# Performance work log

Measured on AMD Instinct MI355X. Metric: run time of the kernel, lower is better.

The kernel has to match this reference:

```python
import jax, jax.numpy as jnp
import numpy as np

N, N_H = 256, 64          # detections per image, humans (permuted to top)
NUM_ITER = 2
E = 1024                   # node_encoding_size == box_feature_size
T_LIS, K_LIS, W_LIS = 8.3, 12.0, 10.0


def lis(x):
    # Low-grade Instance Suppression
    return T_LIS / (1.0 + jnp.exp(K_LIS - W_LIS * x))


def setup_inputs() -> dict:
    key = jax.random.key(0)
    ks = jax.random.split(key, 25)
    s = 0.02  # weight scale keeps sigmoid/relu in a sane range
    rn = lambda k, shape, sc=1.0: jax.random.normal(k, shape, jnp.float32) * sc
    inp = {}
    inp['box_features'] = rn(ks[0], (N, 12544))            # [N, 256*7*7]
    inp['node_spatial'] = rn(ks[1], (N, 1024))             # conv spatial-head output
    inp['scores'] = jax.random.uniform(ks[2], (N,), jnp.float32)
    labels = jax.random.randint(ks[3], (N,), 1, 80)
    inp['labels'] = labels.at[:N_H].set(0)                 # humans (idx 0) on top
    inp['class_mask'] = jax.random.bernoulli(ks[4], 0.2, (80, 117))
    inp['W_bh1'] = rn(ks[5], (12544, 1024), s); inp['b_bh1'] = jnp.zeros((1024,), jnp.float32)
    inp['W_bh2'] = rn(ks[6], (1024, 1024), s);  inp['b_bh2'] = jnp.zeros((1024,), jnp.float32)
    inp['W_sa']  = rn(ks[7], (1024, 1024), s)
    inp['W_a1']  = rn(ks[8], (4096, 2048), s); inp['b_a1'] = jnp.zeros((2048,), jnp.float32)
    inp['W_a2']  = rn(ks[9], (2048, 1024), s); inp['b_a2'] = jnp.zeros((1024,), jnp.float32)
    inp['W_a3']  = rn(ks[10], (1024, 1), s);   inp['b_a3'] = jnp.zeros((1,), jnp.float32)
    inp['W_hm']  = rn(ks[11], (1024, 1024), s); inp['b_hm'] = jnp.zeros((1024,), jnp.float32)
    inp['W_om']  = rn(ks[12], (1024, 1024), s); inp['b_om'] = jnp.zeros((1024,), jnp.float32)
    inp['W_hu']  = rn(ks[13], (2048, 1024), s)
    inp['W_ou']  = rn(ks[14], (2048, 1024), s)
    return inp


def _keep_indices():
    xv, yv = np.meshgrid(np.arange(N_H), np.arange(N), indexing='ij')
    m = (xv != yv).ravel()
    return jnp.asarray(xv.ravel()[m]), jnp.asarray(yv.ravel()[m])


def reference(box_features, node_spatial, scores, W_bh1, b_bh1, W_bh2, b_bh2,
              W_sa, W_a1, b_a1, W_a2, b_a2, W_a3, b_a3,
              W_hm, b_hm, W_om, b_om, W_hu, W_ou, labels, class_mask):
    # box_head: Flatten -> Linear -> ReLU -> Linear -> ReLU
    enc = jax.nn.relu(box_features @ W_bh1 + b_bh1)
    enc = jax.nn.relu(enc @ W_bh2 + b_bh2)                 # [N, E]
    h_enc = enc[:N_H]                                      # [N_H, E]
    h_sp = node_spatial[:N_H]                              # [N_H, 1024]
    # spatial_attention on pairwise spatial differences (fixed across iters)
    diff = node_spatial[None, :, :] - h_sp[:, None, :]     # [N_H, N, 1024]
    h_to_o = jnp.einsum('hnd,de->hne', diff, W_sa)         # Linear, no bias
    o_to_h = -h_to_o
    adj = jnp.ones((N_H, N), enc.dtype)
    for _ in range(NUM_ITER):
        # adjacency MLP + sigmoid over all n_h*n pairs
        hf = jnp.concatenate([h_enc, h_sp], axis=1)        # [N_H, 2048]
        of = jnp.concatenate([enc, node_spatial], axis=1)  # [N, 2048]
        pair_in = jnp.concatenate([
            jnp.broadcast_to(hf[:, None, :], (N_H, N, 2 * E)),
            jnp.broadcast_to(of[None, :, :], (N_H, N, 2 * E))], axis=-1)  # [N_H,N,4096]
        hdn = jax.nn.relu(pair_in @ W_a1 + b_a1)
        hdn = jax.nn.relu(hdn @ W_a2 + b_a2)
        adj = jax.nn.sigmoid((hdn @ W_a3 + b_a3)[..., 0])  # [N_H, N]
        # object -> human messages
        obj_msg = jax.nn.relu(enc @ W_om + b_om)           # [N, R]
        agg_o = (adj[..., None] * (obj_msg[None, :, :] * o_to_h)).sum(1)  # [N_H, R]
        h_enc = jnp.concatenate([h_enc, agg_o], axis=1) @ W_hu            # [N_H, E]
        # human -> object messages
        hum_msg = jax.nn.relu(h_enc @ W_hm + b_hm)         # [N_H, R]
        agg_h = (adj[..., None] * (hum_msg[:, None, :] * h_to_o)).sum(0)  # [N, R]
        enc = jnp.concatenate([enc, agg_h], axis=1) @ W_ou                # [N, E]
    x_keep, y_keep = _keep_indices()                       # [P], P = N_H*N - N_H
    pair_feats = jnp.concatenate([h_enc[x_keep], h_sp[x_keep],
                                  enc[y_keep], node_spatial[y_keep]], axis=1)  # [P, 4096]
    # prior scores: LIS(score_h)*LIS(score_o) scattered to valid target classes
    prod = lis(scores[x_keep]) * lis(scores[y_keep])       # [P]
    prior = prod[:, None] * class_mask[labels[y_keep]].astype(pair_feats.dtype)  # [P, 117]
    prior = adj[x_keep, y_keep][:, None] * prior
    return jnp.concatenate([pair_feats, prior], axis=1)    # [P, 4096+117]
```

## Files before the change

kernel.cpp:

```cpp
#include <hip/hip_runtime.h>

using bf16 = __bf16;
typedef __bf16 bf16x4 __attribute__((ext_vector_type(4)));
typedef __bf16 bf16x8 __attribute__((ext_vector_type(8)));
typedef float  f32x4  __attribute__((ext_vector_type(4)));

#define GST 40

__device__ __forceinline__ float ldf(const void* p, size_t i, int f32) {
    return f32 ? ((const float*)p)[i] : (float)((const bf16*)p)[i];
}
__device__ __forceinline__ bf16x8 ld8(const void* p, size_t i, int f32) {
    bf16x8 r;
    if (f32) {
        f32x4 a = *(const f32x4*)((const float*)p + i);
        f32x4 b = *(const f32x4*)((const float*)p + i + 4);
#pragma unroll
        for (int j = 0; j < 4; ++j) { r[j] = (bf16)a[j]; r[j + 4] = (bf16)b[j]; }
    } else {
        r = *(const bf16x8*)((const bf16*)p + i);
    }
    return r;
}
__device__ __forceinline__ void st1(void* p, size_t i, float v, int f32) {
    if (f32) ((float*)p)[i] = v;
    else     ((bf16*)p)[i] = (bf16)v;
}

__device__ __forceinline__ void gl_lds16(const bf16* g, bf16* l) {
    __builtin_amdgcn_global_load_lds(
        (const __attribute__((address_space(1))) void*)g,
        (__attribute__((address_space(3))) void*)l, 16, 0, 0);
}

__global__ void init_flag(int* __restrict__ dflag) { *dflag = 0; }

__global__ void detect_kernel(const unsigned short* __restrict__ p, int n,
                              int* __restrict__ dflag)
{
    const unsigned int* q = (const unsigned int*)p;
    const int nw = n >> 1;
    int hit = 0;
    for (int i = blockIdx.x * 256 + threadIdx.x; i < nw; i += gridDim.x * 256) {
        unsigned int w = q[i];
        if ((w & 0x7F80u) == 0x7F80u || (w & 0x7F800000u) == 0x7F800000u) hit = 1;
    }
    if (__any(hit) && (threadIdx.x & 63) == 0) atomicOr(dflag, 1);
}

__global__ void cvt_kernel(const void* __restrict__ src, bf16* __restrict__ dst,
                           int n, const int* __restrict__ dflag)
{
    const int f32 = *dflag;
    const int stride = gridDim.x * 256;
    const int nv = n >> 3;
    for (int i = blockIdx.x * 256 + threadIdx.x; i < nv; i += stride) {
        bf16x8 v = ld8(src, (size_t)i * 8, f32);
        *(bf16x8*)(dst + (size_t)i * 8) = v;
    }
}

__global__ void cvt_smalls(const void* b_bh1, const void* b_bh2, const void* b_om,
                           const void* b_hm, const void* b_a1, const void* b_a2,
                           const void* w_a3, const void* b_a3, const void* scores,
                           bf16* __restrict__ smalls, const int* __restrict__ dflag)
{
    const int f32 = *dflag;
    int i = blockIdx.x * 256 + threadIdx.x;
    const void* s; int off;
    if      (i < 1024) { s = b_bh1; off = 0;    }
    else if (i < 2048) { s = b_bh2; off = 1024; }
    else if (i < 3072) { s = b_om;  off = 2048; }
    else if (i < 4096) { s = b_hm;  off = 3072; }
    else if (i < 6144) { s = b_a1;  off = 4096; }
    else if (i < 7168) { s = b_a2;  off = 6144; }
    else if (i < 8192) { s = w_a3;  off = 7168; }
    else if (i < 8193) { s = b_a3;  off = 8192; }
    else if (i >= 8208 && i < 8464) { s = scores; off = 8208; }
    else return;
    smalls[i] = (bf16)ldf(s, i - off, f32);
}

__global__ void transpose_any(const void* __restrict__ W, bf16* __restrict__ Wt,
                              int K, int N, const int* __restrict__ dflag)
{
    __shared__ bf16 tile[32][33];
    const int f32 = *dflag;
    const int n0 = blockIdx.x * 32, k0 = blockIdx.y * 32;
    const int tx = threadIdx.x, ty = threadIdx.y;
#pragma unroll
    for (int i = 0; i < 4; ++i)
        tile[ty + i * 8][tx] = (bf16)ldf(W, (size_t)(k0 + ty + i * 8) * N + n0 + tx, f32);
    __syncthreads();
#pragma unroll
    for (int i = 0; i < 4; ++i)
        Wt[(size_t)(n0 + ty + i * 8) * K + k0 + tx] = tile[tx][ty + i * 8];
}

__global__ __launch_bounds__(256)
void gemm_p(const bf16* __restrict__ A, int lda,
            const void* __restrict__ B, size_t boff, int ldb,
            float* __restrict__ part, int N, int Kc,
            const int* __restrict__ dflag)
{
    __shared__ bf16 As[64 * GST];
    __shared__ bf16 Bs[64 * GST];
    const int f32 = *dflag;
    const int t = threadIdx.x;
    const int l = t & 63;
    const int quad = l >> 4, lr = l & 15;
    const int w = t >> 6, wm = w >> 1, wn = w & 1;
    const int mBlock = blockIdx.y * 64, nBlock = blockIdx.x * 64;
    const int ar = t >> 2, ac = (t & 3) * 8;
    const int kr = t >> 3, nc = (t & 7) * 8;
    const int kBeg = blockIdx.z * Kc;
    const int nIter = Kc >> 5;

    f32x4 acc[2][2] = {};

    bf16x8 avr = *(const bf16x8*)(A + (size_t)(mBlock + ar) * lda + kBeg + ac);
    bf16x8 bvr = ld8(B, boff + (size_t)(kBeg + kr) * ldb + nBlock + nc, f32);

    for (int it = 0; it < nIter; ++it) {
        *(bf16x8*)&As[ar * GST + ac] = avr;
#pragma unroll
        for (int j = 0; j < 8; ++j) {
            int wr = nc + j;
            Bs[wr * GST + (kr ^ (((wr >> 3) & 3) << 3))] = bvr[j];
        }
        __syncthreads();
        if (it + 1 < nIter) {
            int k0 = kBeg + (it + 1) * 32;
            avr = *(const bf16x8*)(A + (size_t)(mBlock + ar) * lda + k0 + ac);
            bvr = ld8(B, boff + (size_t)(k0 + kr) * ldb + nBlock + nc, f32);
        }
        bf16x8 af[2], bfr[2];
#pragma unroll
        for (int mi = 0; mi < 2; ++mi)
            af[mi] = *(const bf16x8*)&As[(wm * 32 + mi * 16 + lr) * GST + quad * 8];
#pragma unroll
        for (int nj = 0; nj < 2; ++nj) {
            int row = wn * 32 + nj * 16 + lr;
            bfr[nj] = *(const bf16x8*)&Bs[row * GST + ((quad * 8) ^ (((row >> 3) & 3) << 3))];
        }
#pragma unroll
        for (int mi = 0; mi < 2; ++mi)
#pragma unroll
            for (int nj = 0; nj < 2; ++nj)
                acc[mi][nj] = __builtin_amdgcn_mfma_f32_16x16x32_bf16(
                    af[mi], bfr[nj], acc[mi][nj], 0, 0, 0);
        __syncthreads();
    }

    float* outp = part + (size_t)blockIdx.z * ((size_t)gridDim.y * 64 * N);
#pragma unroll
    for (int mi = 0; mi < 2; ++mi)
#pragma unroll
        for (int nj = 0; nj < 2; ++nj) {
            int col = nBlock + wn * 32 + nj * 16 + lr;
#pragma unroll
            for (int rr = 0; rr < 4; ++rr) {
                int row = mBlock + wm * 32 + mi * 16 + quad * 4 + rr;
                outp[(size_t)row * N + col] = acc[mi][nj][rr];
            }
        }
}

template<bool RELU, bool BIAS, bool F32OUT>
__global__ void reduce_k(const float* __restrict__ part, int S, int total,
                         const bf16* __restrict__ bias, void* __restrict__ out, int N)
{
    int base = (blockIdx.x * 256 + threadIdx.x) * 4;
    if (base >= total) return;
    f32x4 s = *(const f32x4*)(part + base);
    for (int z = 1; z < S; ++z) {
        f32x4 v = *(const f32x4*)(part + (size_t)z * total + base);
        s[0] += v[0]; s[1] += v[1]; s[2] += v[2]; s[3] += v[3];
    }
    int col = base % N;
#pragma unroll
    for (int j = 0; j < 4; ++j) {
        float v = s[j];
        if (BIAS) v += (float)bias[col + j];
        if (RELU) v = fmaxf(v, 0.f);
        if (F32OUT) ((float*)out)[base + j] = v;
        else        ((bf16*)out)[base + j] = (bf16)v;
    }
}

__global__ void build_pairA(const float* __restrict__ Hb, const float* __restrict__ Op,
                            bf16* __restrict__ A)
{
    const int n = blockIdx.x;
    const int h = blockIdx.y;
    const int k = threadIdx.x * 8;
    const float* hp = Hb + (size_t)h * 2048 + k;
    const float* op = Op + (size_t)n * 2048 + k;
    f32x4 h0 = *(const f32x4*)hp, h1 = *(const f32x4*)(hp + 4);
    f32x4 o0 = *(const f32x4*)op, o1 = *(const f32x4*)(op + 4);
    bf16x8 r;
#pragma unroll
    for (int j = 0; j < 4; ++j) {
        r[j]     = (bf16)fmaxf(h0[j] + o0[j], 0.f);
        r[j + 4] = (bf16)fmaxf(h1[j] + o1[j], 0.f);
    }
    *(bf16x8*)(A + ((size_t)h * 256 + n) * 2048 + k) = r;
}

__global__ __launch_bounds__(256)
void pair_gemm(const bf16* __restrict__ Apg, const bf16* __restrict__ Wt_a2,
               const bf16* __restrict__ b_a2, const bf16* __restrict__ w_a3,
               float* __restrict__ slots)
{
    __shared__ bf16 As[128 * 32];
    __shared__ bf16 Bs[128 * 32];
    const int t = threadIdx.x;
    const int l = t & 63, w = t >> 6;
    const int quad = l >> 4, lr = l & 15;
    const int wm = w >> 1, wn = w & 1;
    const int nb = blockIdx.x, mb = blockIdx.y;
    const int p0 = mb * 128;

    const int grow = w * 16 + (l >> 2);
    const int slot = l & 3;
    const int csrc = slot ^ ((grow >> 1) & 3);
    const bf16* Asrc0 = Apg + (size_t)(p0 + grow) * 2048 + csrc * 8;
    const bf16* Asrc1 = Apg + (size_t)(p0 + 64 + grow) * 2048 + csrc * 8;
    const bf16* Bsrc0 = Wt_a2 + (size_t)(nb * 128 + grow) * 2048 + csrc * 8;
    const bf16* Bsrc1 = Wt_a2 + (size_t)(nb * 128 + 64 + grow) * 2048 + csrc * 8;
    bf16* AsW0 = As + w * 512;
    bf16* AsW1 = As + 2048 + w * 512;
    bf16* BsW0 = Bs + w * 512;
    bf16* BsW1 = Bs + 2048 + w * 512;

    f32x4 acc[4][4] = {};

    for (int k0 = 0; k0 < 2048; k0 += 32) {
        gl_lds16(Asrc0 + k0, AsW0);
        gl_lds16(Asrc1 + k0, AsW1);
        gl_lds16(Bsrc0 + k0, BsW0);
        gl_lds16(Bsrc1 + k0, BsW1);
        __syncthreads();

        bf16x8 af[4], bfr[4];
#pragma unroll
        for (int mi = 0; mi < 4; ++mi) {
            int row = wm * 64 + mi * 16 + lr;
            int sl = quad ^ ((row >> 1) & 3);
            af[mi] = *(const bf16x8*)&As[row * 32 + sl * 8];
        }
#pragma unroll
        for (int nj = 0; nj < 4; ++nj) {
            int row = wn * 64 + nj * 16 + lr;
            int sl = quad ^ ((row >> 1) & 3);
            bfr[nj] = *(const bf16x8*)&Bs[row * 32 + sl * 8];
        }
#pragma unroll
        for (int mi = 0; mi < 4; ++mi)
#pragma unroll
            for (int nj = 0; nj < 4; ++nj)
                acc[mi][nj] = __builtin_amdgcn_mfma_f32_16x16x32_bf16(
                    af[mi], bfr[nj], acc[mi][nj], 0, 0, 0);
        __syncthreads();
    }

    float w3v[4], b2v[4];
#pragma unroll
    for (int nj = 0; nj < 4; ++nj) {
        int col = nb * 128 + wn * 64 + nj * 16 + lr;
        w3v[nj] = (float)w_a3[col];
        b2v[nj] = (float)b_a2[col];
    }
#pragma unroll
    for (int mi = 0; mi < 4; ++mi) {
        f32x4 rs = {0.f, 0.f, 0.f, 0.f};
#pragma unroll
        for (int nj = 0; nj < 4; ++nj)
#pragma unroll
            for (int rr = 0; rr < 4; ++rr)
                rs[rr] += fmaxf(acc[mi][nj][rr] + b2v[nj], 0.f) * w3v[nj];
#pragma unroll
        for (int off = 1; off < 16; off <<= 1) {
            rs[0] += __shfl_xor(rs[0], off);
            rs[1] += __shfl_xor(rs[1], off);
            rs[2] += __shfl_xor(rs[2], off);
            rs[3] += __shfl_xor(rs[3], off);
        }
        if (lr == 0) {
            int p = p0 + wm * 64 + mi * 16 + quad * 4;
            int slot2 = nb * 2 + wn;
            slots[(size_t)(p + 0) * 16 + slot2] = rs[0];
            slots[(size_t)(p + 1) * 16 + slot2] = rs[1];
            slots[(size_t)(p + 2) * 16 + slot2] = rs[2];
            slots[(size_t)(p + 3) * 16 + slot2] = rs[3];
        }
    }
}

__global__ void adj_finalize(const float* __restrict__ slots,
                             const bf16* __restrict__ b_a3, float* __restrict__ adj)
{
    int i = blockIdx.x * 256 + threadIdx.x;
    float s = (float)b_a3[0];
#pragma unroll
    for (int k = 0; k < 16; ++k) s += slots[(size_t)i * 16 + k];
    adj[i] = 1.f / (1.f + expf(-s));
}

__global__ void copy_rows(const bf16* __restrict__ src, int lds_,
                          bf16* __restrict__ dst, int ldd)
{
    int c = blockIdx.x * 256 + threadIdx.x;
    int r = blockIdx.y;
    dst[(size_t)r * ldd + c] = src[(size_t)r * lds_ + c];
}

__global__ void concat2(const bf16* __restrict__ L, const bf16* __restrict__ R,
                        bf16* __restrict__ dst)
{
    int c = blockIdx.x * 256 + threadIdx.x;
    int r = blockIdx.y;
    dst[(size_t)r * 2048 + c] = (c < 1024) ? L[(size_t)r * 1024 + c]
                                           : R[(size_t)r * 1024 + (c - 1024)];
}

__global__ void agg_o_kernel(const float* __restrict__ adj, const bf16* __restrict__ obj_msg,
                             const bf16* __restrict__ nsW, const bf16* __restrict__ h_enc,
                             bf16* __restrict__ out)
{
    int bx = blockIdx.x;
    int h = blockIdx.y;
    int e = (bx & 3) * 256 + threadIdx.x;
    if (bx < 4) {
        out[(size_t)h * 2048 + e] = h_enc[(size_t)h * 1024 + e];
        return;
    }
    float nh = (float)nsW[h * 1024 + e];
    float s = 0.f;
    for (int n = 0; n < 256; ++n) {
        float a  = adj[h * 256 + n];
        float om = (float)obj_msg[n * 1024 + e];
        float nw = (float)nsW[n * 1024 + e];
        s += a * om * (nh - nw);
    }
    out[(size_t)h * 2048 + 1024 + e] = (bf16)s;
}

__global__ void agg_h_kernel(const float* __restrict__ adj, const bf16* __restrict__ hum_msg,
                             const bf16* __restrict__ nsW, const bf16* __restrict__ enc,
                             bf16* __restrict__ out)
{
    int bx = blockIdx.x;
    int n = blockIdx.y;
    int e = (bx & 3) * 256 + threadIdx.x;
    if (bx < 4) {
        out[(size_t)n * 2048 + e] = enc[(size_t)n * 1024 + e];
        return;
    }
    float nn = (float)nsW[n * 1024 + e];
    float s = 0.f;
    for (int h = 0; h < 64; ++h) {
        float a  = adj[h * 256 + n];
        float hm = (float)hum_msg[h * 1024 + e];
        float nw = (float)nsW[h * 1024 + e];
        s += a * hm * (nn - nw);
    }
    out[(size_t)n * 2048 + 1024 + e] = (bf16)s;
}

__global__ void out_kernel(const bf16* __restrict__ h_enc, const bf16* __restrict__ enc,
                           const bf16* __restrict__ nsp_bf, const float* __restrict__ adj,
                           const bf16* __restrict__ scores_bf, const int* __restrict__ labels,
                           const int* __restrict__ cmask, void* __restrict__ out,
                           const int* __restrict__ dflag)
{
    const int f32 = *dflag;
    const int r = blockIdx.x;
    const int x = r / 255;
    const int tt = r % 255;
    const int y = tt + (tt >= x ? 1 : 0);
    const size_t rbase = (size_t)r * 4213;
    const bf16* seg[4] = { h_enc + x * 1024, nsp_bf + x * 1024, enc + y * 1024, nsp_bf + y * 1024 };
    const int t = threadIdx.x;

    float sx = (float)scores_bf[x], sy = (float)scores_bf[y];
    float lx = 8.3f / (1.f + expf(12.f - 10.f * sx));
    float ly = 8.3f / (1.f + expf(12.f - 10.f * sy));
    float pf = adj[x * 256 + y] * lx * ly;
    const int* cm = cmask + labels[y] * 117;

    auto getv = [&](int e) -> float {
        if (e < 4096) return (float)seg[e >> 10][e & 1023];
        return cm[e - 4096] ? pf : 0.f;
    };

    if (f32) {
        float* op = (float*)out + rbase;
        const int ali = (int)((4 - (rbase & 3)) & 3);
        const int nv = (4213 - ali) >> 2;
        for (int vi = t; vi < nv; vi += 256) {
            int e0 = ali + vi * 4;
            f32x4 v = { getv(e0), getv(e0 + 1), getv(e0 + 2), getv(e0 + 3) };
            *(f32x4*)(op + e0) = v;
        }
        if (t < ali) op[t] = getv(t);
        int te = ali + nv * 4;
        if (t < 4213 - te) op[te + t] = getv(te + t);
    } else {
        bf16* op = (bf16*)out + rbase;
        for (int e = t; e < 4213; e += 256) op[e] = (bf16)getv(e);
    }
}

extern "C" void kernel_launch(void* const* d_in, const int* in_sizes, int n_in,
                              void* d_out, int out_size, void* d_ws, size_t ws_size,
                              hipStream_t stream)
{
    (void)in_sizes; (void)n_in; (void)out_size; (void)ws_size;
    const void* box    = d_in[0];
    const void* nsp    = d_in[1];
    const void* scores = d_in[2];
    const int*  labels = (const int*)d_in[3];
    const int*  cmask  = (const int*)d_in[4];
    const void* W_bh1 = d_in[5],  *b_bh1 = d_in[6];
    const void* W_bh2 = d_in[7],  *b_bh2 = d_in[8];
    const void* W_sa  = d_in[9];
    const void* W_a1  = d_in[10], *b_a1  = d_in[11];
    const void* W_a2  = d_in[12], *b_a2  = d_in[13];
    const void* W_a3  = d_in[14], *b_a3  = d_in[15];
    const void* W_hm  = d_in[16], *b_hm  = d_in[17];
    const void* W_om  = d_in[18], *b_om  = d_in[19];
    const void* W_hu  = d_in[20];
    const void* W_ou  = d_in[21];

    char* ws = (char*)d_ws;
    size_t off = 0;
    auto alloc = [&](size_t bytes) -> void* {
        off = (off + 255) & ~(size_t)255;
        void* p = ws + off;
        off += bytes;
        return p;
    };
    int*  dflag   = (int*)alloc(4);
    bf16* box_bf  = (bf16*)alloc((size_t)256 * 12544 * 2);
    bf16* nsp_bf  = (bf16*)alloc((size_t)256 * 1024 * 2);
    bf16* Wt_a2   = (bf16*)alloc((size_t)1024 * 2048 * 2);
    bf16* smalls  = (bf16*)alloc((size_t)8464 * 2);
    bf16* sb_bh1 = smalls,        *sb_bh2 = smalls + 1024;
    bf16* sb_om  = smalls + 2048, *sb_hm  = smalls + 3072;
    bf16* sb_a1  = smalls + 4096, *sb_a2  = smalls + 6144;
    bf16* sw_a3  = smalls + 7168, *sb_a3  = smalls + 8192;
    bf16* sscore = smalls + 8208;
    bf16* t0      = (bf16*)alloc((size_t)256 * 1024 * 2);
    bf16* enc     = (bf16*)alloc((size_t)256 * 1024 * 2);
    bf16* nsW     = (bf16*)alloc((size_t)256 * 1024 * 2);
    bf16* h_enc   = (bf16*)alloc((size_t)64 * 1024 * 2);
    bf16* hf      = (bf16*)alloc((size_t)64 * 2048 * 2);
    bf16* of      = (bf16*)alloc((size_t)256 * 2048 * 2);
    float* Hpart  = (float*)alloc((size_t)64 * 2048 * 4);
    float* Opart  = (float*)alloc((size_t)256 * 2048 * 4);
    float* slots  = (float*)alloc((size_t)16384 * 16 * 4);
    float* adj    = (float*)alloc((size_t)16384 * 4);
    bf16* obj_msg = (bf16*)alloc((size_t)256 * 1024 * 2);
    bf16* hu_in   = (bf16*)alloc((size_t)64 * 2048 * 2);
    bf16* hum_msg = (bf16*)alloc((size_t)64 * 1024 * 2);
    bf16* ou_in   = (bf16*)alloc((size_t)256 * 2048 * 2);
    float* part   = (float*)alloc((size_t)2097152 * 4);
    bf16* A_bf    = (bf16*)alloc((size_t)16384 * 2048 * 2);

    init_flag<<<1, 1, 0, stream>>>(dflag);
    detect_kernel<<<256, 256, 0, stream>>>((const unsigned short*)box, 524288, dflag);

    cvt_kernel<<<1568, 256, 0, stream>>>(box, box_bf, 256 * 12544, dflag);
    cvt_kernel<<<128, 256, 0, stream>>>(nsp, nsp_bf, 256 * 1024, dflag);
    cvt_smalls<<<34, 256, 0, stream>>>(b_bh1, b_bh2, b_om, b_hm, b_a1, b_a2,
                                       W_a3, b_a3, scores, smalls, dflag);

    transpose_any<<<dim3(1024 / 32, 2048 / 32), dim3(32, 8), 0, stream>>>(
        W_a2, Wt_a2, 2048, 1024, dflag);

    gemm_p<<<dim3(16, 4, 8), 256, 0, stream>>>(box_bf, 12544, W_bh1, 0, 1024, part, 1024, 1568, dflag);
    reduce_k<true, true, false><<<dim3(256), 256, 0, stream>>>(part, 8, 262144, sb_bh1, t0, 1024);
    gemm_p<<<dim3(16, 4, 4), 256, 0, stream>>>(t0, 1024, W_bh2, 0, 1024, part, 1024, 256, dflag);
    reduce_k<true, true, false><<<dim3(256), 256, 0, stream>>>(part, 4, 262144, sb_bh2, enc, 1024);
    gemm_p<<<dim3(16, 4, 4), 256, 0, stream>>>(nsp_bf, 1024, W_sa, 0, 1024, part, 1024, 256, dflag);
    reduce_k<false, false, false><<<dim3(256), 256, 0, stream>>>(part, 4, 262144, nullptr, nsW, 1024);
    copy_rows<<<dim3(4, 64), 256, 0, stream>>>(enc, 1024, h_enc, 1024);

    for (int it = 0; it < 2; ++it) {
        concat2<<<dim3(8, 64), 256, 0, stream>>>(h_enc, nsp_bf, hf);
        concat2<<<dim3(8, 256), 256, 0, stream>>>(enc, nsp_bf, of);
        gemm_p<<<dim3(32, 1, 8), 256, 0, stream>>>(hf, 2048, W_a1, 0, 2048, part, 2048, 256, dflag);
        reduce_k<false, true, true><<<dim3(128), 256, 0, stream>>>(part, 8, 131072, sb_a1, Hpart, 2048);
        gemm_p<<<dim3(32, 4, 4), 256, 0, stream>>>(of, 2048, W_a1, (size_t)2048 * 2048, 2048, part, 2048, 512, dflag);
        reduce_k<false, false, true><<<dim3(512), 256, 0, stream>>>(part, 4, 524288, nullptr, Opart, 2048);
        build_pairA<<<dim3(256, 64), 256, 0, stream>>>(Hpart, Opart, A_bf);
        pair_gemm<<<dim3(8, 128), 256, 0, stream>>>(A_bf, Wt_a2, sb_a2, sw_a3, slots);
        adj_finalize<<<dim3(64), 256, 0, stream>>>(slots, sb_a3, adj);
        gemm_p<<<dim3(16, 4, 4), 256, 0, stream>>>(enc, 1024, W_om, 0, 1024, part, 1024, 256, dflag);
        reduce_k<true, true, false><<<dim3(256), 256, 0, stream>>>(part, 4, 262144, sb_om, obj_msg, 1024);
        agg_o_kernel<<<dim3(8, 64), 256, 0, stream>>>(adj, obj_msg, nsW, h_enc, hu_in);
        gemm_p<<<dim3(16, 1, 16), 256, 0, stream>>>(hu_in, 2048, W_hu, 0, 1024, part, 1024, 128, dflag);
        reduce_k<false, false, false><<<dim3(64), 256, 0, stream>>>(part, 16, 65536, nullptr, h_enc, 1024);
        gemm_p<<<dim3(16, 1, 16), 256, 0, stream>>>(h_enc, 1024, W_hm, 0, 1024, part, 1024, 64, dflag);
        reduce_k<true, true, false><<<dim3(64), 256, 0, stream>>>(part, 16, 65536, sb_hm, hum_msg, 1024);
        agg_h_kernel<<<dim3(8, 256), 256, 0, stream>>>(adj, hum_msg, nsW, enc, ou_in);
        gemm_p<<<dim3(16, 4, 4), 256, 0, stream>>>(ou_in, 2048, W_ou, 0, 1024, part, 1024, 512, dflag);
        reduce_k<false, false, false><<<dim3(256), 256, 0, stream>>>(part, 4, 262144, nullptr, enc, 1024);
    }

    out_kernel<<<dim3(16320), 256, 0, stream>>>(
        h_enc, enc, nsp_bf, adj, sscore, labels, cmask, d_out, dflag);
}
```

Baseline: 991.3 us.

## Double-buffer pair GEMM LDS, remap its grid, and write encodings into concat buffers

```diff
diff --git a/kernel.cpp b/kernel.cpp
--- a/kernel.cpp
+++ b/kernel.cpp
@@ -168,7 +168,8 @@
 
 template<bool RELU, bool BIAS, bool F32OUT>
 __global__ void reduce_k(const float* __restrict__ part, int S, int total,
-                         const bf16* __restrict__ bias, void* __restrict__ out, int N)
+                         const bf16* __restrict__ bias, void* __restrict__ out,
+                         int N, int ldd)
 {
     int base = (blockIdx.x * 256 + threadIdx.x) * 4;
     if (base >= total) return;
@@ -177,14 +178,15 @@
         f32x4 v = *(const f32x4*)(part + (size_t)z * total + base);
         s[0] += v[0]; s[1] += v[1]; s[2] += v[2]; s[3] += v[3];
     }
-    int col = base % N;
+    int row = base / N, col = base % N;
+    size_t ob = (size_t)row * ldd + col;
 #pragma unroll
     for (int j = 0; j < 4; ++j) {
         float v = s[j];
         if (BIAS) v += (float)bias[col + j];
         if (RELU) v = fmaxf(v, 0.f);
-        if (F32OUT) ((float*)out)[base + j] = v;
-        else        ((bf16*)out)[base + j] = (bf16)v;
+        if (F32OUT) ((float*)out)[ob + j] = v;
+        else        ((bf16*)out)[ob + j] = (bf16)v;
     }
 }
 
@@ -212,13 +214,14 @@
                const bf16* __restrict__ b_a2, const bf16* __restrict__ w_a3,
                float* __restrict__ slots)
 {
-    __shared__ bf16 As[128 * 32];
-    __shared__ bf16 Bs[128 * 32];
+    __shared__ bf16 As[2][128 * 32];
+    __shared__ bf16 Bs[2][128 * 32];
     const int t = threadIdx.x;
     const int l = t & 63, w = t >> 6;
     const int quad = l >> 4, lr = l & 15;
     const int wm = w >> 1, wn = w & 1;
-    const int nb = blockIdx.x, mb = blockIdx.y;
+    const int nb = blockIdx.y & 7;
+    const int mb = blockIdx.x * 16 + (blockIdx.y >> 3);
     const int p0 = mb * 128;
 
     const int grow = w * 16 + (l >> 2);
@@ -228,32 +231,41 @@
     const bf16* Asrc1 = Apg + (size_t)(p0 + 64 + grow) * 2048 + csrc * 8;
     const bf16* Bsrc0 = Wt_a2 + (size_t)(nb * 128 + grow) * 2048 + csrc * 8;
     const bf16* Bsrc1 = Wt_a2 + (size_t)(nb * 128 + 64 + grow) * 2048 + csrc * 8;
-    bf16* AsW0 = As + w * 512;
-    bf16* AsW1 = As + 2048 + w * 512;
-    bf16* BsW0 = Bs + w * 512;
-    bf16* BsW1 = Bs + 2048 + w * 512;
+    const int woff = w * 512;
 
     f32x4 acc[4][4] = {};
 
-    for (int k0 = 0; k0 < 2048; k0 += 32) {
-        gl_lds16(Asrc0 + k0, AsW0);
-        gl_lds16(Asrc1 + k0, AsW1);
-        gl_lds16(Bsrc0 + k0, BsW0);
-        gl_lds16(Bsrc1 + k0, BsW1);
-        __syncthreads();
-
+    gl_lds16(Asrc0, As[0] + woff);
+    gl_lds16(Asrc1, As[0] + 2048 + woff);
+    gl_lds16(Bsrc0, Bs[0] + woff);
+    gl_lds16(Bsrc1, Bs[0] + 2048 + woff);
+    __syncthreads();
+
+    int cur = 0;
+    for (int kt = 0; kt < 64; ++kt) {
+        if (kt < 63) {
+            int kn = (kt + 1) * 32;
+            bf16* An = As[cur ^ 1];
+            bf16* Bn = Bs[cur ^ 1];
+            gl_lds16(Asrc0 + kn, An + woff);
+            gl_lds16(Asrc1 + kn, An + 2048 + woff);
+            gl_lds16(Bsrc0 + kn, Bn + woff);
+            gl_lds16(Bsrc1 + kn, Bn + 2048 + woff);
+        }
+        const bf16* Ac = As[cur];
+        const bf16* Bc = Bs[cur];
         bf16x8 af[4], bfr[4];
 #pragma unroll
         for (int mi = 0; mi < 4; ++mi) {
             int row = wm * 64 + mi * 16 + lr;
             int sl = quad ^ ((row >> 1) & 3);
-            af[mi] = *(const bf16x8*)&As[row * 32 + sl * 8];
+            af[mi] = *(const bf16x8*)&Ac[row * 32 + sl * 8];
         }
 #pragma unroll
         for (int nj = 0; nj < 4; ++nj) {
             int row = wn * 64 + nj * 16 + lr;
             int sl = quad ^ ((row >> 1) & 3);
-            bfr[nj] = *(const bf16x8*)&Bs[row * 32 + sl * 8];
+            bfr[nj] = *(const bf16x8*)&Bc[row * 32 + sl * 8];
         }
 #pragma unroll
         for (int mi = 0; mi < 4; ++mi)
@@ -262,6 +274,7 @@
                 acc[mi][nj] = __builtin_amdgcn_mfma_f32_16x16x32_bf16(
                     af[mi], bfr[nj], acc[mi][nj], 0, 0, 0);
         __syncthreads();
+        cur ^= 1;
     }
 
     float w3v[4], b2v[4];
@@ -315,24 +328,15 @@
     dst[(size_t)r * ldd + c] = src[(size_t)r * lds_ + c];
 }
 
-__global__ void concat2(const bf16* __restrict__ L, const bf16* __restrict__ R,
-                        bf16* __restrict__ dst)
-{
-    int c = blockIdx.x * 256 + threadIdx.x;
-    int r = blockIdx.y;
-    dst[(size_t)r * 2048 + c] = (c < 1024) ? L[(size_t)r * 1024 + c]
-                                           : R[(size_t)r * 1024 + (c - 1024)];
-}
-
 __global__ void agg_o_kernel(const float* __restrict__ adj, const bf16* __restrict__ obj_msg,
-                             const bf16* __restrict__ nsW, const bf16* __restrict__ h_enc,
+                             const bf16* __restrict__ nsW, const bf16* __restrict__ hf,
                              bf16* __restrict__ out)
 {
     int bx = blockIdx.x;
     int h = blockIdx.y;
     int e = (bx & 3) * 256 + threadIdx.x;
     if (bx < 4) {
-        out[(size_t)h * 2048 + e] = h_enc[(size_t)h * 1024 + e];
+        out[(size_t)h * 2048 + e] = hf[(size_t)h * 2048 + e];
         return;
     }
     float nh = (float)nsW[h * 1024 + e];
@@ -347,14 +351,14 @@
 }
 
 __global__ void agg_h_kernel(const float* __restrict__ adj, const bf16* __restrict__ hum_msg,
-                             const bf16* __restrict__ nsW, const bf16* __restrict__ enc,
+                             const bf16* __restrict__ nsW, const bf16* __restrict__ of,
                              bf16* __restrict__ out)
 {
     int bx = blockIdx.x;
     int n = blockIdx.y;
     int e = (bx & 3) * 256 + threadIdx.x;
     if (bx < 4) {
-        out[(size_t)n * 2048 + e] = enc[(size_t)n * 1024 + e];
+        out[(size_t)n * 2048 + e] = of[(size_t)n * 2048 + e];
         return;
     }
     float nn = (float)nsW[n * 1024 + e];
@@ -368,7 +372,7 @@
     out[(size_t)n * 2048 + 1024 + e] = (bf16)s;
 }
 
-__global__ void out_kernel(const bf16* __restrict__ h_enc, const bf16* __restrict__ enc,
+__global__ void out_kernel(const bf16* __restrict__ hf, const bf16* __restrict__ of,
                            const bf16* __restrict__ nsp_bf, const float* __restrict__ adj,
                            const bf16* __restrict__ scores_bf, const int* __restrict__ labels,
                            const int* __restrict__ cmask, void* __restrict__ out,
@@ -380,7 +384,8 @@
     const int tt = r % 255;
     const int y = tt + (tt >= x ? 1 : 0);
     const size_t rbase = (size_t)r * 4213;
-    const bf16* seg[4] = { h_enc + x * 1024, nsp_bf + x * 1024, enc + y * 1024, nsp_bf + y * 1024 };
+    const bf16* seg[4] = { hf + (size_t)x * 2048, nsp_bf + x * 1024,
+                           of + (size_t)y * 2048, nsp_bf + y * 1024 };
     const int t = threadIdx.x;
 
     float sx = (float)scores_bf[x], sy = (float)scores_bf[y];
@@ -452,9 +457,7 @@
     bf16* sw_a3  = smalls + 7168, *sb_a3  = smalls + 8192;
     bf16* sscore = smalls + 8208;
     bf16* t0      = (bf16*)alloc((size_t)256 * 1024 * 2);
-    bf16* enc     = (bf16*)alloc((size_t)256 * 1024 * 2);
     bf16* nsW     = (bf16*)alloc((size_t)256 * 1024 * 2);
-    bf16* h_enc   = (bf16*)alloc((size_t)64 * 1024 * 2);
     bf16* hf      = (bf16*)alloc((size_t)64 * 2048 * 2);
     bf16* of      = (bf16*)alloc((size_t)256 * 2048 * 2);
     float* Hpart  = (float*)alloc((size_t)64 * 2048 * 4);
@@ -480,35 +483,35 @@
         W_a2, Wt_a2, 2048, 1024, dflag);
 
     gemm_p<<<dim3(16, 4, 8), 256, 0, stream>>>(box_bf, 12544, W_bh1, 0, 1024, part, 1024, 1568, dflag);
-    reduce_k<true, true, false><<<dim3(256), 256, 0, stream>>>(part, 8, 262144, sb_bh1, t0, 1024);
+    reduce_k<true, true, false><<<dim3(256), 256, 0, stream>>>(part, 8, 262144, sb_bh1, t0, 1024, 1024);
     gemm_p<<<dim3(16, 4, 4), 256, 0, stream>>>(t0, 1024, W_bh2, 0, 1024, part, 1024, 256, dflag);
-    reduce_k<true, true, false><<<dim3(256), 256, 0, stream>>>(part, 4, 262144, sb_bh2, enc, 1024);
+    reduce_k<true, true, false><<<dim3(256), 256, 0, stream>>>(part, 4, 262144, sb_bh2, of, 1024, 2048);
     gemm_p<<<dim3(16, 4, 4), 256, 0, stream>>>(nsp_bf, 1024, W_sa, 0, 1024, part, 1024, 256, dflag);
-    reduce_k<false, false, false><<<dim3(256), 256, 0, stream>>>(part, 4, 262144, nullptr, nsW, 1024);
-    copy_rows<<<dim3(4, 64), 256, 0, stream>>>(enc, 1024, h_enc, 1024);
+    reduce_k<false, false, false><<<dim3(256), 256, 0, stream>>>(part, 4, 262144, nullptr, nsW, 1024, 1024);
+    copy_rows<<<dim3(4, 64), 256, 0, stream>>>(of, 2048, hf, 2048);
+    copy_rows<<<dim3(4, 64), 256, 0, stream>>>(nsp_bf, 1024, hf + 1024, 2048);
+    copy_rows<<<dim3(4, 256), 256, 0, stream>>>(nsp_bf, 1024, of + 1024, 2048);
 
     for (int it = 0; it < 2; ++it) {
-        concat2<<<dim3(8, 64), 256, 0, stream>>>(h_enc, nsp_bf, hf);
-        concat2<<<dim3(8, 256), 256, 0, stream>>>(enc, nsp_bf, of);
         gemm_p<<<dim3(32, 1, 8), 256, 0, stream>>>(hf, 2048, W_a1, 0, 2048, part, 2048, 256, dflag);
-        reduce_k<false, true, true><<<dim3(128), 256, 0, stream>>>(part, 8, 131072, sb_a1, Hpart, 2048);
+        reduce_k<false, true, true><<<dim3(128), 256, 0, stream>>>(part, 8, 131072, sb_a1, Hpart, 2048, 2048);
         gemm_p<<<dim3(32, 4, 4), 256, 0, stream>>>(of, 2048, W_a1, (size_t)2048 * 2048, 2048, part, 2048, 512, dflag);
-        reduce_k<false, false, true><<<dim3(512), 256, 0, stream>>>(part, 4, 524288, nullptr, Opart, 2048);
+        reduce_k<false, false, true><<<dim3(512), 256, 0, stream>>>(part, 4, 524288, nullptr, Opart, 2048, 2048);
         build_pairA<<<dim3(256, 64), 256, 0, stream>>>(Hpart, Opart, A_bf);
         pair_gemm<<<dim3(8, 128), 256, 0, stream>>>(A_bf, Wt_a2, sb_a2, sw_a3, slots);
         adj_finalize<<<dim3(64), 256, 0, stream>>>(slots, sb_a3, adj);
-        gemm_p<<<dim3(16, 4, 4), 256, 0, stream>>>(enc, 1024, W_om, 0, 1024, part, 1024, 256, dflag);
-        reduce_k<true, true, false><<<dim3(256), 256, 0, stream>>>(part, 4, 262144, sb_om, obj_msg, 1024);
-        agg_o_kernel<<<dim3(8, 64), 256, 0, stream>>>(adj, obj_msg, nsW, h_enc, hu_in);
+        gemm_p<<<dim3(16, 4, 4), 256, 0, stream>>>(of, 2048, W_om, 0, 1024, part, 1024, 256, dflag);
+        reduce_k<true, true, false><<<dim3(256), 256, 0, stream>>>(part, 4, 262144, sb_om, obj_msg, 1024, 1024);
+        agg_o_kernel<<<dim3(8, 64), 256, 0, stream>>>(adj, obj_msg, nsW, hf, hu_in);
         gemm_p<<<dim3(16, 1, 16), 256, 0, stream>>>(hu_in, 2048, W_hu, 0, 1024, part, 1024, 128, dflag);
-        reduce_k<false, false, false><<<dim3(64), 256, 0, stream>>>(part, 16, 65536, nullptr, h_enc, 1024);
-        gemm_p<<<dim3(16, 1, 16), 256, 0, stream>>>(h_enc, 1024, W_hm, 0, 1024, part, 1024, 64, dflag);
-        reduce_k<true, true, false><<<dim3(64), 256, 0, stream>>>(part, 16, 65536, sb_hm, hum_msg, 1024);
-        agg_h_kernel<<<dim3(8, 256), 256, 0, stream>>>(adj, hum_msg, nsW, enc, ou_in);
+        reduce_k<false, false, false><<<dim3(64), 256, 0, stream>>>(part, 16, 65536, nullptr, hf, 1024, 2048);
+        gemm_p<<<dim3(16, 1, 16), 256, 0, stream>>>(hf, 2048, W_hm, 0, 1024, part, 1024, 64, dflag);
+        reduce_k<true, true, false><<<dim3(64), 256, 0, stream>>>(part, 16, 65536, sb_hm, hum_msg, 1024, 1024);
+        agg_h_kernel<<<dim3(8, 256), 256, 0, stream>>>(adj, hum_msg, nsW, of, ou_in);
         gemm_p<<<dim3(16, 4, 4), 256, 0, stream>>>(ou_in, 2048, W_ou, 0, 1024, part, 1024, 512, dflag);
-        reduce_k<false, false, false><<<dim3(256), 256, 0, stream>>>(part, 4, 262144, nullptr, enc, 1024);
+        reduce_k<false, false, false><<<dim3(256), 256, 0, stream>>>(part, 4, 262144, nullptr, of, 1024, 2048);
     }
 
     out_kernel<<<dim3(16320), 256, 0, stream>>>(
-        h_enc, enc, nsp_bf, adj, sscore, labels, cmask, d_out, dflag);
-}
+        hf, of, nsp_bf, adj, sscore, labels, cmask, d_out, dflag);
+}
```

Result: faster. 966.1 us (-2.5%).
